# Kernel tuning notes

Hardware: AMD Instinct MI355X
Metric: run time of the kernel (lower is better)

Reference implementation:

```python
import jax, jax.numpy as jnp
import numpy as np

EMBED = 1024
HEADS = 16
HEAD_DIM = EMBED // HEADS
FFN = 4096
BSZ = 2
CHUNK = 128
NCHUNK = 16
REG_LEN = CHUNK * NCHUNK   # 2048
SUM_LEN = NCHUNK           # 1 summary token per chunk
NEG = -1e9


def _layer_norm(x, g, b, eps=1e-5):
    mu = x.mean(-1, keepdims=True)
    var = ((x - mu) ** 2).mean(-1, keepdims=True)
    return (x - mu) * jax.lax.rsqrt(var + eps) * g + b


def _build_mask(reg_chunk_ranges, sum_len, reg_len):
    # True = attention allowed. Museformer hierarchical scheme:
    #   rr: reg token attends reg tokens of its OWN chunk, causally
    #   rs: reg token attends summary tokens of STRICTLY EARLIER chunks
    #   sr: summary token of chunk c attends reg tokens of chunk c
    #   ss: causal among summary tokens
    bsz = reg_chunk_ranges.shape[0]
    starts = reg_chunk_ranges[:, :, 0]                       # [B, C]
    t = jnp.arange(reg_len)
    chunk_id = (t[None, :, None] >= starts[:, None, :]).sum(-1) - 1   # [B, R]
    sum_chunk = jnp.arange(sum_len)                          # [S]
    rr = (chunk_id[:, :, None] == chunk_id[:, None, :]) & (t[None, :, None] >= t[None, None, :])
    rs = sum_chunk[None, None, :] < chunk_id[:, :, None]     # [B, R, S]
    sr = chunk_id[:, None, :] == sum_chunk[None, :, None]    # [B, S, R]
    ss = jnp.broadcast_to(sum_chunk[:, None] >= sum_chunk[None, :], (bsz, sum_len, sum_len))
    top = jnp.concatenate([ss, sr], axis=2)
    bot = jnp.concatenate([rs, rr], axis=2)
    return jnp.concatenate([top, bot], axis=1)               # [B, S+R, S+R]


def _forward(x, w_q, w_k, w_v, w_o,
             ln_sa_sum_g, ln_sa_sum_b, ln_sa_reg_g, ln_sa_reg_b,
             sum_fc1_w, sum_fc1_b, sum_fc2_w, sum_fc2_b,
             reg_fc1_w, reg_fc1_b, reg_fc2_w, reg_fc2_b,
             ln_f_sum_g, ln_f_sum_b, ln_f_reg_g, ln_f_reg_b,
             reg_chunk_ranges, sum_len, reg_len):
    bsz, total, d = x.shape
    # --- self-attention block (pre-norm, separate LN for sum/reg parts) ---
    hs = _layer_norm(x[:, :sum_len], ln_sa_sum_g, ln_sa_sum_b)
    hr = _layer_norm(x[:, sum_len:], ln_sa_reg_g, ln_sa_reg_b)
    h = jnp.concatenate([hs, hr], axis=1)
    q = (h @ w_q.T).reshape(bsz, total, HEADS, HEAD_DIM)
    k = (h @ w_k.T).reshape(bsz, total, HEADS, HEAD_DIM)
    v = (h @ w_v.T).reshape(bsz, total, HEADS, HEAD_DIM)
    scores = jnp.einsum('bqhd,bkhd->bhqk', q, k) * (HEAD_DIM ** -0.5)
    mask = _build_mask(reg_chunk_ranges, sum_len, reg_len)   # [B, T, T] bool
    scores = jnp.where(mask[:, None], scores, NEG)
    attn = jax.nn.softmax(scores, axis=-1)
    ctx = jnp.einsum('bhqk,bkhd->bqhd', attn, v).reshape(bsz, total, d)
    x = x + ctx @ w_o.T
    # --- FFN block (pre-norm, separate LN/FFN for sum/reg parts) ---
    fs = _layer_norm(x[:, :sum_len], ln_f_sum_g, ln_f_sum_b)
    fs = jax.nn.relu(fs @ sum_fc1_w.T + sum_fc1_b) @ sum_fc2_w.T + sum_fc2_b
    fr = _layer_norm(x[:, sum_len:], ln_f_reg_g, ln_f_reg_b)
    fr = jax.nn.relu(fr @ reg_fc1_w.T + reg_fc1_b) @ reg_fc2_w.T + reg_fc2_b
    return x + jnp.concatenate([fs, fr], axis=1)


def setup_inputs() -> dict:
    key = jax.random.key(0)
    ks = jax.random.split(key, 12)
    s = 0.02
    total = SUM_LEN + REG_LEN
    starts = (np.arange(NCHUNK) * CHUNK).astype(np.int32)
    ranges = np.stack([starts, starts + CHUNK], axis=-1)     # [C, 2]
    reg_chunk_ranges = jnp.asarray(np.broadcast_to(ranges, (BSZ, NCHUNK, 2)).copy())
    d = dict(
        x=jax.random.normal(ks[0], (BSZ, total, EMBED), jnp.float32),
        w_q=jax.random.normal(ks[1], (EMBED, EMBED), jnp.float32) * s,
        w_k=jax.random.normal(ks[2], (EMBED, EMBED), jnp.float32) * s,
        w_v=jax.random.normal(ks[3], (EMBED, EMBED), jnp.float32) * s,
        w_o=jax.random.normal(ks[4], (EMBED, EMBED), jnp.float32) * s,
        ln_sa_sum_g=jnp.ones((EMBED,)), ln_sa_sum_b=jnp.zeros((EMBED,)),
        ln_sa_reg_g=jnp.ones((EMBED,)), ln_sa_reg_b=jnp.zeros((EMBED,)),
        sum_fc1_w=jax.random.normal(ks[5], (FFN, EMBED), jnp.float32) * s,
        sum_fc1_b=jnp.zeros((FFN,)),
        sum_fc2_w=jax.random.normal(ks[6], (EMBED, FFN), jnp.float32) * s,
        sum_fc2_b=jnp.zeros((EMBED,)),
        reg_fc1_w=jax.random.normal(ks[7], (FFN, EMBED), jnp.float32) * s,
        reg_fc1_b=jnp.zeros((FFN,)),
        reg_fc2_w=jax.random.normal(ks[8], (EMBED, FFN), jnp.float32) * s,
        reg_fc2_b=jnp.zeros((EMBED,)),
        ln_f_sum_g=jnp.ones((EMBED,)), ln_f_sum_b=jnp.zeros((EMBED,)),
        ln_f_reg_g=jnp.ones((EMBED,)), ln_f_reg_b=jnp.zeros((EMBED,)),
        reg_chunk_ranges=reg_chunk_ranges,
        sum_len=SUM_LEN,
        reg_len=REG_LEN,
    )
    return d


def reference(x, w_q, w_k, w_v, w_o,
              ln_sa_sum_g, ln_sa_sum_b, ln_sa_reg_g, ln_sa_reg_b,
              sum_fc1_w, sum_fc1_b, sum_fc2_w, sum_fc2_b,
              reg_fc1_w, reg_fc1_b, reg_fc2_w, reg_fc2_b,
              ln_f_sum_g, ln_f_sum_b, ln_f_reg_g, ln_f_reg_b,
              reg_chunk_ranges, sum_len, reg_len):
    return _forward(x, w_q, w_k, w_v, w_o,
                    ln_sa_sum_g, ln_sa_sum_b, ln_sa_reg_g, ln_sa_reg_b,
                    sum_fc1_w, sum_fc1_b, sum_fc2_w, sum_fc2_b,
                    reg_fc1_w, reg_fc1_b, reg_fc2_w, reg_fc2_b,
                    ln_f_sum_g, ln_f_sum_b, ln_f_reg_g, ln_f_reg_b,
                    reg_chunk_ranges, sum_len, reg_len)
```

## Files before the change

### kernel.cpp

```cpp
#include <hip/hip_runtime.h>
#include <stdint.h>

typedef __attribute__((ext_vector_type(8))) short short8;
typedef __attribute__((ext_vector_type(4))) float f32x4;

__device__ __forceinline__ float bf2f(short s) {
    union { unsigned u; float f; } c;
    c.u = ((unsigned)(unsigned short)s) << 16;
    return c.f;
}
__device__ __forceinline__ short f2bf(float f) {
    union { float f; unsigned u; } c; c.f = f;
    unsigned u = c.u + 0x7fffu + ((c.u >> 16) & 1u);
    return (short)(u >> 16);
}
__device__ __forceinline__ void gll16(const short* g, short* l) {
    __builtin_amdgcn_global_load_lds(
        (const __attribute__((address_space(1))) unsigned int*)g,
        (__attribute__((address_space(3))) unsigned int*)l, 16, 0, 0);
}

__global__ __launch_bounds__(256) void cvt_w(
    const float* __restrict__ wq, const float* __restrict__ wk,
    const float* __restrict__ wv, const float* __restrict__ wo,
    const float* __restrict__ f1s, const float* __restrict__ f2s,
    const float* __restrict__ f1r, const float* __restrict__ f2r,
    short* __restrict__ dst)
{
    size_t i = ((size_t)blockIdx.x * 256 + threadIdx.x) * 4;
    const float* src; size_t off;
    if (i < 4194304) {
        int seg = (int)(i >> 20);
        src = seg == 0 ? wq : seg == 1 ? wk : seg == 2 ? wv : wo;
        off = i & 1048575;
    } else {
        size_t ii = i - 4194304;
        int seg = (int)(ii >> 22);
        src = seg == 0 ? f1s : seg == 1 ? f2s : seg == 2 ? f1r : f2r;
        off = ii & 4194303;
    }
    float4 v = *(const float4*)(src + off);
    short4 o;
    o.x = f2bf(v.x); o.y = f2bf(v.y); o.z = f2bf(v.z); o.w = f2bf(v.w);
    *(short4*)(dst + i) = o;
}

template<int PHASE>
__global__ __launch_bounds__(256) void ln_k(
    const float* __restrict__ xin, const short* __restrict__ Pw, float* __restrict__ x1out,
    const float* __restrict__ g_sum, const float* __restrict__ b_sum,
    const float* __restrict__ g_reg, const float* __restrict__ b_reg,
    short* __restrict__ out_all, short* __restrict__ out_s, short* __restrict__ out_r)
{
    int row = blockIdx.x;
    int b = row / 2064, t = row - b * 2064;
    int tid = threadIdx.x;
    int c = tid * 4;
    size_t base = (size_t)row * 1024 + c;
    float4 v = *(const float4*)(xin + base);
    if (PHASE == 1) {
#pragma unroll
        for (int z = 0; z < 4; ++z) {
            short4 p = *(const short4*)(Pw + (size_t)z * 4227072 + base);
            v.x += bf2f(p.x); v.y += bf2f(p.y);
            v.z += bf2f(p.z); v.w += bf2f(p.w);
        }
        *(float4*)(x1out + base) = v;
    }
    float s = v.x + v.y + v.z + v.w;
#pragma unroll
    for (int off = 1; off < 64; off <<= 1) s += __shfl_xor(s, off);
    __shared__ float red[8];
    if ((tid & 63) == 0) red[tid >> 6] = s;
    __syncthreads();
    float mu = (red[0] + red[1] + red[2] + red[3]) * (1.0f / 1024.0f);
    float a0 = v.x - mu, a1 = v.y - mu, a2 = v.z - mu, a3 = v.w - mu;
    float qq = a0 * a0 + a1 * a1 + a2 * a2 + a3 * a3;
#pragma unroll
    for (int off = 1; off < 64; off <<= 1) qq += __shfl_xor(qq, off);
    if ((tid & 63) == 0) red[4 + (tid >> 6)] = qq;
    __syncthreads();
    float var = (red[4] + red[5] + red[6] + red[7]) * (1.0f / 1024.0f);
    float rs = rsqrtf(var + 1e-5f);
    const float* g  = (t < 16) ? g_sum : g_reg;
    const float* be = (t < 16) ? b_sum : b_reg;
    short4 o;
    o.x = f2bf(a0 * rs * g[c]     + be[c]);
    o.y = f2bf(a1 * rs * g[c + 1] + be[c + 1]);
    o.z = f2bf(a2 * rs * g[c + 2] + be[c + 2]);
    o.w = f2bf(a3 * rs * g[c + 3] + be[c + 3]);
    short* dst;
    if (PHASE == 0) dst = out_all + (size_t)row * 1024;
    else dst = (t < 16) ? (out_s + ((size_t)b * 16 + t) * 1024)
                        : (out_r + ((size_t)b * 2048 + (t - 16)) * 1024);
    *(short4*)(dst + c) = o;
}

template<int MODE>
__global__ __launch_bounds__(512) void gemm256(
    const short* __restrict__ A, int M, int K, int klen,
    const short* __restrict__ B0, const short* __restrict__ B1, const short* __restrict__ B2,
    const float* __restrict__ bias,
    void* __restrict__ o0, void* __restrict__ o1, void* __restrict__ o2, int seg)
{
    const int tid = threadIdx.x;
    const int w = tid >> 6, l = tid & 63;
    const int lr = l & 15, lh = l >> 4;
    const int m0 = blockIdx.x * 256;
    int ntile = blockIdx.y, nsel = 0;
    const short* B = B0;
    if (MODE == 0) { nsel = ntile >> 2; ntile &= 3; B = nsel == 0 ? B0 : (nsel == 1 ? B1 : B2); }
    const int n0 = ntile * 256;
    const int wm = w >> 2, wn = w & 3;
    const int kbase = blockIdx.z * klen;

    __shared__ __align__(16) short As[2 * 8192];
    __shared__ __align__(16) short Bs[2 * 8192];

    const int srow = w * 32 + (l >> 2);
    const int scol = (((l & 3) ^ ((l >> 3) & 3))) * 8;
    int ar0 = m0 + srow;      if (ar0 > M - 1) ar0 = M - 1;
    int ar1 = m0 + srow + 16; if (ar1 > M - 1) ar1 = M - 1;
    const short* ga0 = A + (size_t)ar0 * K + scol + kbase;
    const short* ga1 = A + (size_t)ar1 * K + scol + kbase;
    const short* gb0 = B + (size_t)(n0 + srow) * K + scol + kbase;
    const short* gb1 = B + (size_t)(n0 + srow + 16) * K + scol + kbase;
    const int lofs = (w * 32) * 32;

    const int cbrd = (lh ^ ((lr >> 1) & 3)) * 8;

    f32x4 acc[8][4];
#pragma unroll
    for (int m = 0; m < 8; ++m)
#pragma unroll
        for (int n = 0; n < 4; ++n) acc[m][n] = (f32x4){0.f, 0.f, 0.f, 0.f};

    auto STAGE = [&](int j, int buf) {
        const int k0 = j * 32;
        short* a = As + buf * 8192 + lofs;
        short* b = Bs + buf * 8192 + lofs;
        gll16(ga0 + k0, a);
        gll16(ga1 + k0, a + 512);
        gll16(gb0 + k0, b);
        gll16(gb1 + k0, b + 512);
    };

    const int nk = klen >> 5;
    STAGE(0, 0);
    for (int t = 0; t < nk; ++t) {
        __syncthreads();
        const int cur = (t & 1);
        if (t + 1 < nk) STAGE(t + 1, cur ^ 1);
        const int co = cur << 13;
        short8 bfr[4];
#pragma unroll
        for (int n = 0; n < 4; ++n)
            bfr[n] = *(const short8*)(Bs + co + (wn * 64 + n * 16 + lr) * 32 + cbrd);
#pragma unroll
        for (int m = 0; m < 8; ++m) {
            short8 af = *(const short8*)(As + co + (wm * 128 + m * 16 + lr) * 32 + cbrd);
#pragma unroll
            for (int n = 0; n < 4; ++n)
                acc[m][n] = __builtin_amdgcn_mfma_f32_16x16x32_bf16(af, bfr[n], acc[m][n], 0, 0, 0);
        }
    }

#pragma unroll
    for (int m = 0; m < 8; ++m) {
#pragma unroll
        for (int n = 0; n < 4; ++n) {
            int gc = n0 + wn * 64 + n * 16 + lr;
#pragma unroll
            for (int j = 0; j < 4; ++j) {
                int gr = m0 + wm * 128 + m * 16 + lh * 4 + j;
                if (gr >= M) continue;
                float val = acc[m][n][j];
                if (MODE == 0) {
                    short* o = (short*)(nsel == 0 ? o0 : (nsel == 1 ? o1 : o2));
                    o[(size_t)gr * 1024 + gc] = f2bf(val);
                } else if (MODE == 2) {
                    val += bias[gc];
                    val = val > 0.f ? val : 0.f;
                    ((short*)o0)[(size_t)gr * 4096 + gc] = f2bf(val);
                } else {
                    short* P = (short*)o0 + (size_t)blockIdx.z * (size_t)seg;
                    P[(size_t)gr * 1024 + gc] = f2bf(val);
                }
            }
        }
    }
}

template<int MODE>
__global__ __launch_bounds__(256) void gemm_bt(
    const short* __restrict__ A, int M, int K, int klen,
    const short* __restrict__ B0,
    const float* __restrict__ bias,
    void* __restrict__ o0, int seg)
{
    const int tid = threadIdx.x;
    const int w = tid >> 6, l = tid & 63;
    const int lr = l & 15, lh = l >> 4;
    const int m0 = blockIdx.x * 128;
    const int n0 = blockIdx.y * 128;
    const short* B = B0;
    const int wr = (w >> 1) * 64, wc = (w & 1) * 64;
    const int kbase = blockIdx.z * klen;

    __shared__ __align__(16) short As[2 * 4096];
    __shared__ __align__(16) short Bs[2 * 4096];

    const int srow = w * 32 + (l >> 2);
    const int scol = (((l & 3) ^ ((l >> 3) & 3))) * 8;
    int ar0 = m0 + srow;      if (ar0 > M - 1) ar0 = M - 1;
    int ar1 = m0 + srow + 16; if (ar1 > M - 1) ar1 = M - 1;
    const short* ga0 = A + (size_t)ar0 * K + scol + kbase;
    const short* ga1 = A + (size_t)ar1 * K + scol + kbase;
    const short* gb0 = B + (size_t)(n0 + srow) * K + scol + kbase;
    const short* gb1 = B + (size_t)(n0 + srow + 16) * K + scol + kbase;
    const int lofs = (w * 32) * 32;
    const int cbrd = (lh ^ ((lr >> 1) & 3)) * 8;

    f32x4 acc[4][4];
#pragma unroll
    for (int m = 0; m < 4; ++m)
#pragma unroll
        for (int n = 0; n < 4; ++n) acc[m][n] = (f32x4){0.f, 0.f, 0.f, 0.f};

    auto STAGE = [&](int j, int buf) {
        const int k0 = j * 32;
        short* a = As + buf * 4096 + lofs;
        short* b = Bs + buf * 4096 + lofs;
        gll16(ga0 + k0, a);
        gll16(ga1 + k0, a + 512);
        gll16(gb0 + k0, b);
        gll16(gb1 + k0, b + 512);
    };

    const int nk = klen >> 5;
    STAGE(0, 0);
    for (int t = 0; t < nk; ++t) {
        __syncthreads();
        const int cur = (t & 1);
        if (t + 1 < nk) STAGE(t + 1, cur ^ 1);
        const int co = cur << 12;
        short8 af[4], bfr[4];
#pragma unroll
        for (int m = 0; m < 4; ++m)
            af[m] = *(const short8*)(As + co + (wr + m * 16 + lr) * 32 + cbrd);
#pragma unroll
        for (int n = 0; n < 4; ++n)
            bfr[n] = *(const short8*)(Bs + co + (wc + n * 16 + lr) * 32 + cbrd);
#pragma unroll
        for (int m = 0; m < 4; ++m)
#pragma unroll
            for (int n = 0; n < 4; ++n)
                acc[m][n] = __builtin_amdgcn_mfma_f32_16x16x32_bf16(af[m], bfr[n], acc[m][n], 0, 0, 0);
    }

#pragma unroll
    for (int m = 0; m < 4; ++m) {
#pragma unroll
        for (int n = 0; n < 4; ++n) {
            int gc = n0 + wc + n * 16 + lr;
#pragma unroll
            for (int j = 0; j < 4; ++j) {
                int gr = m0 + wr + m * 16 + lh * 4 + j;
                if (gr >= M) continue;
                float val = acc[m][n][j];
                if (MODE == 1) {
                    float* P = (float*)o0 + (size_t)blockIdx.z * (size_t)seg;
                    P[(size_t)gr * 1024 + gc] = val;
                } else {
                    val += bias[gc];
                    val = val > 0.f ? val : 0.f;
                    ((short*)o0)[(size_t)gr * 4096 + gc] = f2bf(val);
                }
            }
        }
    }
}

__global__ __launch_bounds__(256) void reduce_f2reg(
    const float* __restrict__ x1, const short* __restrict__ P,
    const float* __restrict__ bias, float* __restrict__ out)
{
    size_t i = ((size_t)blockIdx.x * 256 + threadIdx.x) * 4;
    int gr = (int)(i >> 10), c = (int)(i & 1023);
    size_t g = (size_t)((gr >> 11) * 2064 + 16 + (gr & 2047)) * 1024 + c;
    float4 r  = *(const float4*)(x1 + g);
    float4 bb = *(const float4*)(bias + c);
    float ox = r.x + bb.x, oy = r.y + bb.y, oz = r.z + bb.z, ow = r.w + bb.w;
#pragma unroll
    for (int z = 0; z < 4; ++z) {
        short4 p = *(const short4*)(P + (size_t)z * 4194304 + i);
        ox += bf2f(p.x); oy += bf2f(p.y); oz += bf2f(p.z); ow += bf2f(p.w);
    }
    float4 o; o.x = ox; o.y = oy; o.z = oz; o.w = ow;
    *(float4*)(out + g) = o;
}

__global__ __launch_bounds__(256) void reduce_f2sum(
    const float* __restrict__ x1, const float* __restrict__ P,
    const float* __restrict__ bias, float* __restrict__ out)
{
    int i = (blockIdx.x * 256 + threadIdx.x) * 4;
    int gr = i >> 10, c = i & 1023;
    size_t g = (size_t)((gr >> 4) * 2064 + (gr & 15)) * 1024 + c;
    float4 r  = *(const float4*)(x1 + g);
    float4 bb = *(const float4*)(bias + c);
    float ox = r.x + bb.x, oy = r.y + bb.y, oz = r.z + bb.z, ow = r.w + bb.w;
#pragma unroll
    for (int s = 0; s < 16; ++s) {
        float4 p = *(const float4*)(P + s * 32768 + i);
        ox += p.x; oy += p.y; oz += p.z; ow += p.w;
    }
    float4 o; o.x = ox; o.y = oy; o.z = oz; o.w = ow;
    *(float4*)(out + g) = o;
}

__global__ __launch_bounds__(256) void attn_reg(
    const short* __restrict__ q, const short* __restrict__ k,
    const short* __restrict__ v, short* __restrict__ ctx)
{
    __shared__ __align__(16) short Pl[128 * 168];
    __shared__ __align__(16) short Vt[64 * 168];
    short* Kl = Pl;

    const int tid = threadIdx.x;
    const int w = tid >> 6, l = tid & 63, lr = l & 15, lh = l >> 4;
    const int c = blockIdx.x, h = blockIdx.y, b = blockIdx.z;
    const int hc = h * 64;
    const size_t rowq0 = (size_t)b * 2064 + 16 + (size_t)c * 128;

    for (int ch = tid; ch < 1152; ch += 256) {
        int row = ch >> 3, kk = (ch & 7) << 3;
        size_t grow = (row < 16) ? ((size_t)b * 2064 + row) : (rowq0 + row - 16);
        *(int4*)(Kl + row * 72 + kk) = *(const int4*)(k + grow * 1024 + hc + kk);
    }
    for (int ch = tid; ch < 1152; ch += 256) {
        int j = ch % 144, db = ch / 144;
        size_t grow = (j < 16) ? ((size_t)b * 2064 + j) : (rowq0 + j - 16);
        short8 dv = *(const short8*)(v + grow * 1024 + hc + db * 8);
#pragma unroll
        for (int i = 0; i < 8; ++i) Vt[(db * 8 + i) * 168 + j] = dv[i];
    }
    for (int idx = tid; idx < 1024; idx += 256) {
        int d = idx >> 4, jj = 144 + (idx & 15);
        Vt[d * 168 + jj] = 0;
    }
    __syncthreads();

    short8 qf[2][2];
#pragma unroll
    for (int m = 0; m < 2; ++m) {
        size_t grow = rowq0 + w * 32 + m * 16 + lr;
#pragma unroll
        for (int ks = 0; ks < 2; ++ks)
            qf[m][ks] = *(const short8*)(q + grow * 1024 + hc + ks * 32 + lh * 8);
    }

    f32x4 s[2][9];
#pragma unroll
    for (int m = 0; m < 2; ++m)
#pragma unroll
        for (int n = 0; n < 9; ++n) s[m][n] = (f32x4){0.f, 0.f, 0.f, 0.f};
#pragma unroll
    for (int n = 0; n < 9; ++n) {
        const short* kr = Kl + (n * 16 + lr) * 72;
        short8 k0 = *(const short8*)(kr + lh * 8);
        short8 k1 = *(const short8*)(kr + 32 + lh * 8);
        s[0][n] = __builtin_amdgcn_mfma_f32_16x16x32_bf16(qf[0][0], k0, s[0][n], 0, 0, 0);
        s[0][n] = __builtin_amdgcn_mfma_f32_16x16x32_bf16(qf[0][1], k1, s[0][n], 0, 0, 0);
        s[1][n] = __builtin_amdgcn_mfma_f32_16x16x32_bf16(qf[1][0], k0, s[1][n], 0, 0, 0);
        s[1][n] = __builtin_amdgcn_mfma_f32_16x16x32_bf16(qf[1][1], k1, s[1][n], 0, 0, 0);
    }

    float inv_[2][4];
#pragma unroll
    for (int m = 0; m < 2; ++m) {
#pragma unroll
        for (int j = 0; j < 4; ++j) {
            int p = w * 32 + m * 16 + lh * 4 + j;
            float best = -1e30f;
            float e[9];
#pragma unroll
            for (int n = 0; n < 9; ++n) {
                int kk = n * 16 + lr;
                bool vis = (kk < 16) ? (kk < c) : (kk - 16 <= p);
                float val = vis ? s[m][n][j] * 0.125f : -1e30f;
                e[n] = val;
                best = fmaxf(best, val);
            }
#pragma unroll
            for (int off = 1; off < 16; off <<= 1) best = fmaxf(best, __shfl_xor(best, off));
            float sm = 0.f;
#pragma unroll
            for (int n = 0; n < 9; ++n) {
                float ex = __expf(e[n] - best);
                s[m][n][j] = ex;
                sm += ex;
            }
#pragma unroll
            for (int off = 1; off < 16; off <<= 1) sm += __shfl_xor(sm, off);
            inv_[m][j] = 1.0f / sm;
        }
    }

    __syncthreads();
#pragma unroll
    for (int m = 0; m < 2; ++m)
#pragma unroll
        for (int n = 0; n < 9; ++n)
#pragma unroll
            for (int j = 0; j < 4; ++j)
                Pl[(w * 32 + m * 16 + lh * 4 + j) * 168 + n * 16 + lr] = f2bf(s[m][n][j]);
    for (int idx = l; idx < 512; idx += 64) {
        int rr = idx >> 4, kkp = 144 + (idx & 15);
        Pl[(w * 32 + rr) * 168 + kkp] = 0;
    }
    __syncthreads();

    f32x4 dacc[2][4];
#pragma unroll
    for (int m = 0; m < 2; ++m)
#pragma unroll
        for (int n = 0; n < 4; ++n) dacc[m][n] = (f32x4){0.f, 0.f, 0.f, 0.f};
#pragma unroll
    for (int ks = 0; ks < 5; ++ks) {
        int kk0 = ks * 32;
        short8 pa[2];
#pragma unroll
        for (int m = 0; m < 2; ++m)
            pa[m] = *(const short8*)(Pl + (w * 32 + m * 16 + lr) * 168 + kk0 + lh * 8);
#pragma unroll
        for (int n = 0; n < 4; ++n) {
            short8 vb = *(const short8*)(Vt + (n * 16 + lr) * 168 + kk0 + lh * 8);
            dacc[0][n] = __builtin_amdgcn_mfma_f32_16x16x32_bf16(pa[0], vb, dacc[0][n], 0, 0, 0);
            dacc[1][n] = __builtin_amdgcn_mfma_f32_16x16x32_bf16(pa[1], vb, dacc[1][n], 0, 0, 0);
        }
    }

#pragma unroll
    for (int m = 0; m < 2; ++m)
#pragma unroll
        for (int n = 0; n < 4; ++n)
#pragma unroll
            for (int j = 0; j < 4; ++j) {
                int p = w * 32 + m * 16 + lh * 4 + j;
                ctx[(rowq0 + p) * 1024 + hc + n * 16 + lr] = f2bf(dacc[m][n][j] * inv_[m][j]);
            }
}

__global__ __launch_bounds__(64) void attn_sum(
    const short* __restrict__ q, const short* __restrict__ k,
    const short* __restrict__ v, short* __restrict__ ctx)
{
    int idx = blockIdx.x;
    int b = idx >> 8, h = (idx >> 4) & 15, s = idx & 15;
    int l = threadIdx.x;
    int hc = h * 64;
    size_t qrow = (size_t)b * 2064 + s;
    __shared__ float qv[64];
    __shared__ float pp[192];
    qv[l] = bf2f(q[qrow * 1024 + hc + l]);
    __syncthreads();
    float sc[3];
#pragma unroll
    for (int i = 0; i < 3; ++i) {
        int j = l + i * 64;
        float t = -1e30f;
        if (j < 144 && (j >= 16 || j <= s)) {
            size_t kr = (j < 16) ? ((size_t)b * 2064 + j)
                                 : ((size_t)b * 2064 + 16 + (size_t)s * 128 + (j - 16));
            const short* kp = k + kr * 1024 + hc;
            float acc = 0.f;
            for (int d = 0; d < 64; ++d) acc += qv[d] * bf2f(kp[d]);
            t = acc * 0.125f;
        }
        sc[i] = t;
    }
    float mx = fmaxf(sc[0], fmaxf(sc[1], sc[2]));
#pragma unroll
    for (int off = 1; off < 64; off <<= 1) mx = fmaxf(mx, __shfl_xor(mx, off));
    float sm = 0.f;
#pragma unroll
    for (int i = 0; i < 3; ++i) {
        float ex = (sc[i] > -1e29f) ? __expf(sc[i] - mx) : 0.f;
        pp[l + i * 64] = ex;
        sm += ex;
    }
#pragma unroll
    for (int off = 1; off < 64; off <<= 1) sm += __shfl_xor(sm, off);
    __syncthreads();
    float invs = 1.0f / sm;
    float acc = 0.f;
    for (int j = 0; j < 144; ++j) {
        float pj = pp[j];
        size_t vr = (j < 16) ? ((size_t)b * 2064 + j)
                             : ((size_t)b * 2064 + 16 + (size_t)s * 128 + (j - 16));
        acc += pj * bf2f(v[vr * 1024 + hc + l]);
    }
    ctx[qrow * 1024 + hc + l] = f2bf(acc * invs);
}

extern "C" void kernel_launch(void* const* d_in, const int* in_sizes, int n_in,
                              void* d_out, int out_size, void* d_ws, size_t ws_size,
                              hipStream_t stream) {
    const float* x    = (const float*)d_in[0];
    const float* wq   = (const float*)d_in[1];
    const float* wk   = (const float*)d_in[2];
    const float* wv   = (const float*)d_in[3];
    const float* wo   = (const float*)d_in[4];
    const float* lsg  = (const float*)d_in[5];
    const float* lsb  = (const float*)d_in[6];
    const float* lrg  = (const float*)d_in[7];
    const float* lrb  = (const float*)d_in[8];
    const float* sf1w = (const float*)d_in[9];
    const float* sf1b = (const float*)d_in[10];
    const float* sf2w = (const float*)d_in[11];
    const float* sf2b = (const float*)d_in[12];
    const float* rf1w = (const float*)d_in[13];
    const float* rf1b = (const float*)d_in[14];
    const float* rf2w = (const float*)d_in[15];
    const float* rf2b = (const float*)d_in[16];
    const float* fsg  = (const float*)d_in[17];
    const float* fsb  = (const float*)d_in[18];
    const float* frg  = (const float*)d_in[19];
    const float* frb  = (const float*)d_in[20];
    float* out = (float*)d_out;

    char* ws = (char*)d_ws;
    short* wbf   = (short*)ws;
    short* wq_b  = wbf;
    short* wk_b  = wbf + 1048576;
    short* wv_b  = wbf + 2097152;
    short* wo_b  = wbf + 3145728;
    short* f1s_b = wbf + 4194304;
    short* f2s_b = wbf + 8388608;
    short* f1r_b = wbf + 12582912;
    short* f2r_b = wbf + 16777216;
    short* h_all = (short*)(ws + 41943040);
    short* qb   = (short*)(ws + 50397184);
    short* kb   = qb + 4227072;
    short* vb   = kb + 4227072;
    short* ctxb = vb + 4227072;
    short* Pwo  = (short*)(ws + 41943040);
    float* x1   = (float*)(ws + 84213760);
    short* h2_reg = (short*)ws;
    short* h2_sum = (short*)(ws + 75759616);
    short* f1_reg = (short*)(ws + 41943040);
    short* f1_sum = (short*)(ws + 75825152);
    float* Psum   = (float*)(ws + 8388608);
    short* Pf2    = (short*)ws;

    cvt_w<<<20480, 256, 0, stream>>>(wq, wk, wv, wo, sf1w, sf2w, rf1w, rf2w, wbf);
    ln_k<0><<<4128, 256, 0, stream>>>(x, nullptr, nullptr, lsg, lsb, lrg, lrb,
                                      h_all, nullptr, nullptr);
    gemm256<0><<<dim3(17, 12, 1), 512, 0, stream>>>(h_all, 4128, 1024, 1024,
        wq_b, wk_b, wv_b, nullptr, qb, kb, vb, 0);
    attn_reg<<<dim3(16, 16, 2), 256, 0, stream>>>(qb, kb, vb, ctxb);
    attn_sum<<<512, 64, 0, stream>>>(qb, kb, vb, ctxb);
    gemm256<3><<<dim3(17, 4, 4), 512, 0, stream>>>(ctxb, 4128, 1024, 256,
        wo_b, nullptr, nullptr, nullptr, Pwo, nullptr, nullptr, 4227072);
    ln_k<1><<<4128, 256, 0, stream>>>(x, Pwo, x1, fsg, fsb, frg, frb,
                                      nullptr, h2_sum, h2_reg);
    gemm256<2><<<dim3(16, 16, 1), 512, 0, stream>>>(h2_reg, 4096, 1024, 1024,
        f1r_b, nullptr, nullptr, rf1b, f1_reg, nullptr, nullptr, 0);
    gemm_bt<2><<<dim3(1, 32, 1), 256, 0, stream>>>(h2_sum, 32, 1024, 1024,
        f1s_b, sf1b, f1_sum, 0);
    gemm_bt<1><<<dim3(1, 8, 16), 256, 0, stream>>>(f1_sum, 32, 4096, 256,
        f2s_b, nullptr, Psum, 32768);
    reduce_f2sum<<<32, 256, 0, stream>>>(x1, Psum, sf2b, out);
    gemm256<3><<<dim3(16, 4, 4), 512, 0, stream>>>(f1_reg, 4096, 4096, 1024,
        f2r_b, nullptr, nullptr, nullptr, Pf2, nullptr, nullptr, 4194304);
    reduce_f2reg<<<4096, 256, 0, stream>>>(x1, Pf2, rf2b, out);
}
```

Measured before the change: 315.3 us.

## Rewrite main GEMM as 8-phase pipelined kernel with BK=64 and prioritized MFMA

Replaces the 256x256 GEMM main loop with a k-step of 64 split into four phases. Each phase issues part of the next tile's global-to-LDS loads, then runs MFMAs at raised wave priority, with explicit vmcnt waits and barriers in between. This overlaps memory traffic with compute at a finer grain and halves the number of k-iterations. The Wo projection split-K also drops from 4 to 2, so the LN kernel sums two partials instead of four. The cost is 128KB of LDS per block and more complex manual synchronisation, and the launch bound of two blocks per CU may not be reachable with that LDS use.

```diff
diff --git a/kernel.cpp b/kernel.cpp
--- a/kernel.cpp
+++ b/kernel.cpp
@@ -19,6 +19,7 @@
         (const __attribute__((address_space(1))) unsigned int*)g,
         (__attribute__((address_space(3))) unsigned int*)l, 16, 0, 0);
 }
+#define MFMA(a, b, c) __builtin_amdgcn_mfma_f32_16x16x32_bf16((a), (b), (c), 0, 0, 0)
 
 __global__ __launch_bounds__(256) void cvt_w(
     const float* __restrict__ wq, const float* __restrict__ wk,
@@ -60,7 +61,7 @@
     float4 v = *(const float4*)(xin + base);
     if (PHASE == 1) {
 #pragma unroll
-        for (int z = 0; z < 4; ++z) {
+        for (int z = 0; z < 2; ++z) {
             short4 p = *(const short4*)(Pw + (size_t)z * 4227072 + base);
             v.x += bf2f(p.x); v.y += bf2f(p.y);
             v.z += bf2f(p.z); v.w += bf2f(p.w);
@@ -97,7 +98,7 @@
 }
 
 template<int MODE>
-__global__ __launch_bounds__(512) void gemm256(
+__global__ __launch_bounds__(512, 2) void gemm8p(
     const short* __restrict__ A, int M, int K, int klen,
     const short* __restrict__ B0, const short* __restrict__ B1, const short* __restrict__ B2,
     const float* __restrict__ bias,
@@ -114,20 +115,18 @@
     const int wm = w >> 2, wn = w & 3;
     const int kbase = blockIdx.z * klen;
 
-    __shared__ __align__(16) short As[2 * 8192];
-    __shared__ __align__(16) short Bs[2 * 8192];
-
-    const int srow = w * 32 + (l >> 2);
-    const int scol = (((l & 3) ^ ((l >> 3) & 3))) * 8;
-    int ar0 = m0 + srow;      if (ar0 > M - 1) ar0 = M - 1;
-    int ar1 = m0 + srow + 16; if (ar1 > M - 1) ar1 = M - 1;
-    const short* ga0 = A + (size_t)ar0 * K + scol + kbase;
-    const short* ga1 = A + (size_t)ar1 * K + scol + kbase;
-    const short* gb0 = B + (size_t)(n0 + srow) * K + scol + kbase;
-    const short* gb1 = B + (size_t)(n0 + srow + 16) * K + scol + kbase;
-    const int lofs = (w * 32) * 32;
-
-    const int cbrd = (lh ^ ((lr >> 1) & 3)) * 8;
+    __shared__ __align__(16) short L[2 * 32768];
+
+    const int srow = tid >> 2;
+    const int scb  = (tid & 3) ^ (srow & 3);
+    int ar0 = m0 + srow;        if (ar0 > M - 1) ar0 = M - 1;
+    int ar1 = m0 + srow + 128;  if (ar1 > M - 1) ar1 = M - 1;
+    const short* gA0 = A + (size_t)ar0 * K + kbase + scb * 8;
+    const short* gA1 = A + (size_t)ar1 * K + kbase + scb * 8;
+    const short* gB0 = B + (size_t)(n0 + srow) * K + kbase + scb * 8;
+    const short* gB1 = B + (size_t)(n0 + srow + 128) * K + kbase + scb * 8;
+    const int wofs = w * 512;
+    const int cbrd = (lh ^ (lr & 3)) * 8;
 
     f32x4 acc[8][4];
 #pragma unroll
@@ -135,34 +134,94 @@
 #pragma unroll
         for (int n = 0; n < 4; ++n) acc[m][n] = (f32x4){0.f, 0.f, 0.f, 0.f};
 
-    auto STAGE = [&](int j, int buf) {
-        const int k0 = j * 32;
-        short* a = As + buf * 8192 + lofs;
-        short* b = Bs + buf * 8192 + lofs;
-        gll16(ga0 + k0, a);
-        gll16(ga1 + k0, a + 512);
-        gll16(gb0 + k0, b);
-        gll16(gb1 + k0, b + 512);
+    auto STG = [&](int tt, int s, bool isB) {
+        const int off = (tt & 1) * 32768 + s * 16384 + (isB ? 8192 : 0);
+        const int gk  = tt * 64 + s * 32;
+        if (!isB) {
+            gll16(gA0 + gk, L + off + wofs);
+            gll16(gA1 + gk, L + off + 4096 + wofs);
+        } else {
+            gll16(gB0 + gk, L + off + wofs);
+            gll16(gB1 + gk, L + off + 4096 + wofs);
+        }
     };
 
-    const int nk = klen >> 5;
-    STAGE(0, 0);
-    for (int t = 0; t < nk; ++t) {
-        __syncthreads();
-        const int cur = (t & 1);
-        if (t + 1 < nk) STAGE(t + 1, cur ^ 1);
-        const int co = cur << 13;
-        short8 bfr[4];
-#pragma unroll
-        for (int n = 0; n < 4; ++n)
-            bfr[n] = *(const short8*)(Bs + co + (wn * 64 + n * 16 + lr) * 32 + cbrd);
+    const int nt = klen >> 6;
+    STG(0, 0, false); STG(0, 0, true); STG(0, 1, false); STG(0, 1, true);
+
+    const int arow = wm * 128, brow = wn * 64;
+
+    for (int t = 0; t < nt; ++t) {
+        const int buf = (t & 1) * 32768;
+        const short* LA0 = L + buf;
+        const short* LB0 = L + buf + 8192;
+        const short* LA1 = L + buf + 16384;
+        const short* LB1 = L + buf + 24576;
+
+        asm volatile("s_waitcnt vmcnt(4)" ::: "memory");
+        __builtin_amdgcn_s_barrier();
+        asm volatile("" ::: "memory");
+        if (t + 1 < nt) STG(t + 1, 0, false);
+        short8 a0[8];
+#pragma unroll
+        for (int m = 0; m < 8; ++m)
+            a0[m] = *(const short8*)(LA0 + (arow + m * 16 + lr) * 32 + cbrd);
+        short8 b0 = *(const short8*)(LB0 + (brow + lr) * 32 + cbrd);
+        short8 b1 = *(const short8*)(LB0 + (brow + 16 + lr) * 32 + cbrd);
+        __builtin_amdgcn_s_setprio(1);
 #pragma unroll
         for (int m = 0; m < 8; ++m) {
-            short8 af = *(const short8*)(As + co + (wm * 128 + m * 16 + lr) * 32 + cbrd);
-#pragma unroll
-            for (int n = 0; n < 4; ++n)
-                acc[m][n] = __builtin_amdgcn_mfma_f32_16x16x32_bf16(af, bfr[n], acc[m][n], 0, 0, 0);
-        }
+            acc[m][0] = MFMA(a0[m], b0, acc[m][0]);
+            acc[m][1] = MFMA(a0[m], b1, acc[m][1]);
+        }
+        __builtin_amdgcn_s_setprio(0);
+
+        asm volatile("" ::: "memory");
+        __builtin_amdgcn_s_barrier();
+        asm volatile("" ::: "memory");
+        if (t + 1 < nt) STG(t + 1, 0, true);
+        short8 b2 = *(const short8*)(LB0 + (brow + 32 + lr) * 32 + cbrd);
+        short8 b3 = *(const short8*)(LB0 + (brow + 48 + lr) * 32 + cbrd);
+        __builtin_amdgcn_s_setprio(1);
+#pragma unroll
+        for (int m = 0; m < 8; ++m) {
+            acc[m][2] = MFMA(a0[m], b2, acc[m][2]);
+            acc[m][3] = MFMA(a0[m], b3, acc[m][3]);
+        }
+        __builtin_amdgcn_s_setprio(0);
+
+        if (t + 1 < nt) asm volatile("s_waitcnt vmcnt(4)" ::: "memory");
+        else            asm volatile("s_waitcnt vmcnt(0)" ::: "memory");
+        __builtin_amdgcn_s_barrier();
+        asm volatile("" ::: "memory");
+        if (t + 1 < nt) STG(t + 1, 1, false);
+        short8 a1[8];
+#pragma unroll
+        for (int m = 0; m < 8; ++m)
+            a1[m] = *(const short8*)(LA1 + (arow + m * 16 + lr) * 32 + cbrd);
+        short8 c0 = *(const short8*)(LB1 + (brow + lr) * 32 + cbrd);
+        short8 c1 = *(const short8*)(LB1 + (brow + 16 + lr) * 32 + cbrd);
+        __builtin_amdgcn_s_setprio(1);
+#pragma unroll
+        for (int m = 0; m < 8; ++m) {
+            acc[m][0] = MFMA(a1[m], c0, acc[m][0]);
+            acc[m][1] = MFMA(a1[m], c1, acc[m][1]);
+        }
+        __builtin_amdgcn_s_setprio(0);
+
+        asm volatile("" ::: "memory");
+        __builtin_amdgcn_s_barrier();
+        asm volatile("" ::: "memory");
+        if (t + 1 < nt) STG(t + 1, 1, true);
+        short8 c2 = *(const short8*)(LB1 + (brow + 32 + lr) * 32 + cbrd);
+        short8 c3 = *(const short8*)(LB1 + (brow + 48 + lr) * 32 + cbrd);
+        __builtin_amdgcn_s_setprio(1);
+#pragma unroll
+        for (int m = 0; m < 8; ++m) {
+            acc[m][2] = MFMA(a1[m], c2, acc[m][2]);
+            acc[m][3] = MFMA(a1[m], c3, acc[m][3]);
+        }
+        __builtin_amdgcn_s_setprio(0);
     }
 
 #pragma unroll
@@ -255,7 +314,7 @@
         for (int m = 0; m < 4; ++m)
 #pragma unroll
             for (int n = 0; n < 4; ++n)
-                acc[m][n] = __builtin_amdgcn_mfma_f32_16x16x32_bf16(af[m], bfr[n], acc[m][n], 0, 0, 0);
+                acc[m][n] = MFMA(af[m], bfr[n], acc[m][n]);
     }
 
 #pragma unroll
@@ -370,10 +429,10 @@
         const short* kr = Kl + (n * 16 + lr) * 72;
         short8 k0 = *(const short8*)(kr + lh * 8);
         short8 k1 = *(const short8*)(kr + 32 + lh * 8);
-        s[0][n] = __builtin_amdgcn_mfma_f32_16x16x32_bf16(qf[0][0], k0, s[0][n], 0, 0, 0);
-        s[0][n] = __builtin_amdgcn_mfma_f32_16x16x32_bf16(qf[0][1], k1, s[0][n], 0, 0, 0);
-        s[1][n] = __builtin_amdgcn_mfma_f32_16x16x32_bf16(qf[1][0], k0, s[1][n], 0, 0, 0);
-        s[1][n] = __builtin_amdgcn_mfma_f32_16x16x32_bf16(qf[1][1], k1, s[1][n], 0, 0, 0);
+        s[0][n] = MFMA(qf[0][0], k0, s[0][n]);
+        s[0][n] = MFMA(qf[0][1], k1, s[0][n]);
+        s[1][n] = MFMA(qf[1][0], k0, s[1][n]);
+        s[1][n] = MFMA(qf[1][1], k1, s[1][n]);
     }
 
     float inv_[2][4];
@@ -436,8 +495,8 @@
 #pragma unroll
         for (int n = 0; n < 4; ++n) {
             short8 vb = *(const short8*)(Vt + (n * 16 + lr) * 168 + kk0 + lh * 8);
-            dacc[0][n] = __builtin_amdgcn_mfma_f32_16x16x32_bf16(pa[0], vb, dacc[0][n], 0, 0, 0);
-            dacc[1][n] = __builtin_amdgcn_mfma_f32_16x16x32_bf16(pa[1], vb, dacc[1][n], 0, 0, 0);
+            dacc[0][n] = MFMA(pa[0], vb, dacc[0][n]);
+            dacc[1][n] = MFMA(pa[1], vb, dacc[1][n]);
         }
     }
 
@@ -557,22 +616,22 @@
     cvt_w<<<20480, 256, 0, stream>>>(wq, wk, wv, wo, sf1w, sf2w, rf1w, rf2w, wbf);
     ln_k<0><<<4128, 256, 0, stream>>>(x, nullptr, nullptr, lsg, lsb, lrg, lrb,
                                       h_all, nullptr, nullptr);
-    gemm256<0><<<dim3(17, 12, 1), 512, 0, stream>>>(h_all, 4128, 1024, 1024,
+    gemm8p<0><<<dim3(17, 12, 1), 512, 0, stream>>>(h_all, 4128, 1024, 1024,
         wq_b, wk_b, wv_b, nullptr, qb, kb, vb, 0);
     attn_reg<<<dim3(16, 16, 2), 256, 0, stream>>>(qb, kb, vb, ctxb);
     attn_sum<<<512, 64, 0, stream>>>(qb, kb, vb, ctxb);
-    gemm256<3><<<dim3(17, 4, 4), 512, 0, stream>>>(ctxb, 4128, 1024, 256,
+    gemm8p<3><<<dim3(17, 4, 2), 512, 0, stream>>>(ctxb, 4128, 1024, 512,
         wo_b, nullptr, nullptr, nullptr, Pwo, nullptr, nullptr, 4227072);
     ln_k<1><<<4128, 256, 0, stream>>>(x, Pwo, x1, fsg, fsb, frg, frb,
                                       nullptr, h2_sum, h2_reg);
-    gemm256<2><<<dim3(16, 16, 1), 512, 0, stream>>>(h2_reg, 4096, 1024, 1024,
+    gemm8p<2><<<dim3(16, 16, 1), 512, 0, stream>>>(h2_reg, 4096, 1024, 1024,
         f1r_b, nullptr, nullptr, rf1b, f1_reg, nullptr, nullptr, 0);
     gemm_bt<2><<<dim3(1, 32, 1), 256, 0, stream>>>(h2_sum, 32, 1024, 1024,
         f1s_b, sf1b, f1_sum, 0);
     gemm_bt<1><<<dim3(1, 8, 16), 256, 0, stream>>>(f1_sum, 32, 4096, 256,
         f2s_b, nullptr, Psum, 32768);
     reduce_f2sum<<<32, 256, 0, stream>>>(x1, Psum, sf2b, out);
-    gemm256<3><<<dim3(16, 4, 4), 512, 0, stream>>>(f1_reg, 4096, 4096, 1024,
+    gemm8p<3><<<dim3(16, 4, 4), 512, 0, stream>>>(f1_reg, 4096, 4096, 1024,
         f2r_b, nullptr, nullptr, nullptr, Pf2, nullptr, nullptr, 4194304);
     reduce_f2reg<<<4096, 256, 0, stream>>>(x1, Pf2, rf2b, out);
 }
```

New measurement: 288.8 us. 8.4% less time.
